# Optimization experiments

Measured on AMD Instinct MI355X. Metric: run time of the kernel, lower is better.

## Reference

```python
import jax, jax.numpy as jnp
import numpy as np
import math

D_MODEL = 1024
NUM_HEADS = 16
HEAD_DIM = D_MODEL // NUM_HEADS
B, T = 2, 2048


def _linear_params(key, d_in, d_out):
    kw, kb = jax.random.split(key)
    s = 1.0 / math.sqrt(d_in)
    W = jax.random.uniform(kw, (d_in, d_out), jnp.float32, -s, s)
    b = jax.random.uniform(kb, (d_out,), jnp.float32, -s, s)
    return W, b


def setup_inputs() -> dict:
    key = jax.random.key(0)
    ks = jax.random.split(key, 10)
    x_real = jax.random.normal(ks[0], (B, T, D_MODEL), jnp.float32)
    x_imag = jax.random.normal(ks[1], (B, T, D_MODEL), jnp.float32)
    Wqr, bqr = _linear_params(ks[2], D_MODEL, D_MODEL)
    Wqi, bqi = _linear_params(ks[3], D_MODEL, D_MODEL)
    Wkr, bkr = _linear_params(ks[4], D_MODEL, D_MODEL)
    Wki, bki = _linear_params(ks[5], D_MODEL, D_MODEL)
    Wvr, bvr = _linear_params(ks[6], D_MODEL, D_MODEL)
    Wvi, bvi = _linear_params(ks[7], D_MODEL, D_MODEL)
    Wor, bor = _linear_params(ks[8], D_MODEL, D_MODEL)
    Woi, boi = _linear_params(ks[9], D_MODEL, D_MODEL)
    return dict(x_real=x_real, x_imag=x_imag,
                Wqr=Wqr, bqr=bqr, Wqi=Wqi, bqi=bqi,
                Wkr=Wkr, bkr=bkr, Wki=Wki, bki=bki,
                Wvr=Wvr, bvr=bvr, Wvi=Wvi, bvi=bvi,
                Wor=Wor, bor=bor, Woi=Woi, boi=boi)


def _heads(x):
    # (B,T,C) -> (B,H,T,Dh)
    b, t, _ = x.shape
    return x.reshape(b, t, NUM_HEADS, HEAD_DIM).transpose(0, 2, 1, 3)


def reference(x_real, x_imag,
              Wqr, bqr, Wqi, bqi, Wkr, bkr, Wki, bki,
              Wvr, bvr, Wvi, bvi, Wor, bor, Woi, boi):
    b, t, c = x_real.shape
    # NOTE: first two qr/qi assignments in the torch forward are dead code;
    # effective math is below.
    qr = _heads(x_real @ Wqr + bqr)
    qi = _heads(x_imag @ Wqi + bqi)
    kr = _heads(x_real @ Wkr + bkr)
    ki = _heads(x_imag @ Wki + bki)
    vr = _heads(x_real @ Wvr + bvr)
    vi = _heads(x_imag @ Wvi + bvi)
    # Re(Q K^H) score: Qr*Kr + Qi*Ki, scaled
    score = (jnp.einsum('bhtd,bhsd->bhts', qr, kr)
             + jnp.einsum('bhtd,bhsd->bhts', qi, ki)) / math.sqrt(HEAD_DIM)
    causal = jnp.triu(jnp.ones((t, t), dtype=bool), k=1)  # True above diagonal
    score = jnp.where(causal[None, None], -jnp.inf, score)
    attn = jax.nn.softmax(score, axis=-1)
    out_r = jnp.einsum('bhts,bhsd->bhtd', attn, vr).transpose(0, 2, 1, 3).reshape(b, t, c)
    out_i = jnp.einsum('bhts,bhsd->bhtd', attn, vi).transpose(0, 2, 1, 3).reshape(b, t, c)
    final_r = out_r @ Wor + bor
    final_i = out_i @ Woi + boi
    return (final_r, final_i)
```

## Files before the change

### kernel.cpp

```cpp
#include <hip/hip_runtime.h>
#include <hip/hip_bf16.h>


typedef __attribute__((ext_vector_type(8))) __bf16 bf16x8;
typedef __attribute__((ext_vector_type(4))) float f32x4;
typedef unsigned short u16;

#define L2E 1.44269504088896340736f

__device__ __forceinline__ void gl2lds16(const void* g, void* l) {
  __builtin_amdgcn_global_load_lds(
      (const __attribute__((address_space(1))) unsigned int*)g,
      (__attribute__((address_space(3))) unsigned int*)l, 16, 0, 0);
}

__device__ __forceinline__ u16 f2bf(float f) {
  union { float f; unsigned u; } v;
  v.f = f;
  unsigned r = v.u + 0x7FFFu + ((v.u >> 16) & 1u);
  return (u16)(r >> 16);
}

__global__ void cvt_bf16(const float* __restrict__ in, u16* __restrict__ out, int n) {
  int stride = gridDim.x * blockDim.x * 4;
  for (int i = (blockIdx.x * blockDim.x + threadIdx.x) * 4; i < n; i += stride) {
    float4 v = *(const float4*)(in + i);
    ushort4 o;
    o.x = f2bf(v.x); o.y = f2bf(v.y); o.z = f2bf(v.z); o.w = f2bf(v.w);
    *(ushort4*)(out + i) = o;
  }
}

struct WPtrs { const float* w[8]; };

__global__ void cvt_w_t(WPtrs ptrs, u16* __restrict__ out) {
  __shared__ float tile[32][33];
  const float* W = ptrs.w[blockIdx.z];
  u16* o = out + ((size_t)blockIdx.z << 20);
  int tx = threadIdx.x & 31, ty = threadIdx.x >> 5;
  int bx = blockIdx.x * 32, by = blockIdx.y * 32;
#pragma unroll
  for (int k = 0; k < 4; k++) {
    int r = by + ty + k * 8;
    tile[ty + k * 8][tx] = W[(size_t)r * 1024 + bx + tx];
  }
  __syncthreads();
#pragma unroll
  for (int k = 0; k < 4; k++) {
    int n = bx + ty + k * 8;
    o[(size_t)n * 1024 + by + tx] = f2bf(tile[tx][ty + k * 8]);
  }
}

struct GemmArgs {
  const u16* A[6];
  const u16* Wt[6];
  const float* bias[6];
  void* dst[6];
  int off[6];
  float scale[6];
};

template <int MODE>
__global__ __launch_bounds__(256, 2) void gemm_bf16(GemmArgs args) {
  const int z = blockIdx.z;
  const u16* __restrict__ A = args.A[z];
  const u16* __restrict__ Bt = args.Wt[z];
  const float* __restrict__ bias = args.bias[z];
  const int brow = blockIdx.x * 128;
  const int bcol = blockIdx.y * 128;

  __shared__ u16 lA[2][128 * 32];
  __shared__ u16 lB[2][128 * 32];

  const int tid = threadIdx.x;
  const int w = tid >> 6, lane = tid & 63;
  const int wrow = (w >> 1) * 64, wcol = (w & 1) * 64;

  f32x4 acc[4][4] = {};

  auto stage = [&](int buf, int t) {
    int k0 = t * 32;
#pragma unroll
    for (int s = 0; s < 2; s++) {
      int q = w * 2 + s;
      int lr = q * 16 + (lane >> 2);
      int csrc = (lane & 3) ^ ((lr >> 1) & 3);
      gl2lds16(A + (size_t)(brow + lr) * 1024 + k0 + csrc * 8, &lA[buf][q * 512]);
    }
#pragma unroll
    for (int s = 0; s < 2; s++) {
      int q = w * 2 + s;
      int lr = q * 16 + (lane >> 2);
      int csrc = (lane & 3) ^ ((lr >> 1) & 3);
      gl2lds16(Bt + (size_t)(bcol + lr) * 1024 + k0 + csrc * 8, &lB[buf][q * 512]);
    }
  };

  stage(0, 0);
  __syncthreads();

  int buf = 0;
  for (int t = 0; t < 32; t++) {
    if (t + 1 < 32) stage(buf ^ 1, t + 1);
    bf16x8 a[4], b[4];
#pragma unroll
    for (int i = 0; i < 4; i++) {
      int row = wrow + i * 16 + (lane & 15);
      int cs = (lane >> 4) ^ ((row >> 1) & 3);
      a[i] = *(const bf16x8*)&lA[buf][row * 32 + cs * 8];
      int col = wcol + i * 16 + (lane & 15);
      int cs2 = (lane >> 4) ^ ((col >> 1) & 3);
      b[i] = *(const bf16x8*)&lB[buf][col * 32 + cs2 * 8];
    }
#pragma unroll
    for (int i = 0; i < 4; i++)
#pragma unroll
      for (int j = 0; j < 4; j++)
        acc[i][j] = __builtin_amdgcn_mfma_f32_16x16x32_bf16(a[i], b[j], acc[i][j], 0, 0, 0);
    __syncthreads();
    buf ^= 1;
  }

  const int off = args.off[z];
  const float scl = args.scale[z];
#pragma unroll
  for (int i = 0; i < 4; i++)
#pragma unroll
    for (int j = 0; j < 4; j++)
#pragma unroll
      for (int r = 0; r < 4; r++) {
        int grow = brow + wrow + i * 16 + (lane >> 4) * 4 + r;
        int gcol = bcol + wcol + j * 16 + (lane & 15);
        float v = (acc[i][j][r] + bias[gcol]) * scl;
        if (MODE == 0) {
          ((float*)args.dst[z])[(size_t)grow * 1024 + gcol] = v;
        } else {
          int bb = grow >> 11, tt = grow & 2047;
          int h = gcol >> 6, dh = gcol & 63;
          ((u16*)args.dst[z])[(((size_t)(bb * 16 + h) * 2048 + tt) << 7) + off + dh] = f2bf(v);
        }
      }
}

__global__ void transpose_v(const u16* __restrict__ Vc, u16* __restrict__ Vt) {
  __shared__ u16 tile[64 * 64];
  const int bh = blockIdx.z, t0 = blockIdx.x * 64, d0 = blockIdx.y * 64;
  const int tid = threadIdx.x;
  const int tl = tid >> 3, c = tid & 7;
#pragma unroll
  for (int hh = 0; hh < 2; hh++) {
    int t = tl + hh * 32;
    int sc = c ^ (t & 7) ^ ((t >> 3) & 7);
    *(bf16x8*)&tile[t * 64 + sc * 8] =
        *(const bf16x8*)&Vc[((size_t)bh * 2048 + t0 + t) * 128 + d0 + c * 8];
  }
  __syncthreads();
#pragma unroll
  for (int hh = 0; hh < 2; hh++) {
    int d = tl + hh * 32;
    bf16x8 v;
#pragma unroll
    for (int j = 0; j < 8; j++) {
      int t = c * 8 + j;
      int sc = (d >> 3) ^ (t & 7) ^ ((t >> 3) & 7);
      v[j] = ((const __bf16*)tile)[t * 64 + sc * 8 + (d & 7)];
    }
    *(bf16x8*)&Vt[((size_t)bh * 128 + d0 + d) * 2048 + t0 + c * 8] = v;
  }
}

__global__ __launch_bounds__(256, 2) void attn_kernel(
    const u16* __restrict__ Q, const u16* __restrict__ K, const u16* __restrict__ Vt,
    u16* __restrict__ Or, u16* __restrict__ Oi) {
  const int bh = blockIdx.x;
  const int ii = (int)gridDim.y - 1 - (int)blockIdx.y;
  const int tid = threadIdx.x, w = tid >> 6, lane = tid & 63;
  const int ql = lane & 15, hi = lane >> 4;
  const int b = bh >> 4, h = bh & 15;

  __shared__ u16 lK[2][64 * 128];
  __shared__ u16 lV[2][128 * 64];
  __shared__ u16 lP[4][16 * 64];

  const int qrow0 = ii * 64 + w * 16;
  const int q = qrow0 + ql;

  bf16x8 qf[4];
#pragma unroll
  for (int kk = 0; kk < 4; kk++)
    qf[kk] = *(const bf16x8*)(Q + ((size_t)bh * 2048 + q) * 128 + kk * 32 + hi * 8);

  f32x4 o[8] = {};
  float m = -__builtin_inff(), l = 0.f;

  const int ntiles = ii + 1;

  auto stageKV = [&](int buf, int jt) {
#pragma unroll
    for (int s = 0; s < 4; s++) {
      int seg = w * 4 + s;
      int srow = seg * 4 + (lane >> 4);
      int csrc = (lane & 15) ^ (srow & 15);
      gl2lds16(K + ((size_t)bh * 2048 + jt * 64 + srow) * 128 + csrc * 8, &lK[buf][seg * 512]);
    }
#pragma unroll
    for (int s = 0; s < 4; s++) {
      int seg = w * 4 + s;
      int dv = seg * 8 + (lane >> 3);
      int csrc = (lane & 7) ^ (dv & 7);
      gl2lds16(Vt + ((size_t)bh * 128 + dv) * 2048 + jt * 64 + csrc * 8, &lV[buf][seg * 512]);
    }
  };

  stageKV(0, 0);
  __syncthreads();

  int buf = 0;
  for (int jt = 0; jt < ntiles; jt++) {
    if (jt + 1 < ntiles) stageKV(buf ^ 1, jt + 1);

    f32x4 s[4] = {};
    __builtin_amdgcn_s_setprio(1);
#pragma unroll
    for (int kk = 0; kk < 4; kk++) {
#pragma unroll
      for (int j = 0; j < 4; j++) {
        int sl = j * 16 + ql;
        int cs = (kk * 4 + hi) ^ (sl & 15);
        bf16x8 kf = *(const bf16x8*)&lK[buf][sl * 128 + cs * 8];
        s[j] = __builtin_amdgcn_mfma_f32_16x16x32_bf16(kf, qf[kk], s[j], 0, 0, 0);
      }
    }
    __builtin_amdgcn_s_setprio(0);

    if (jt == ii) {
#pragma unroll
      for (int j = 0; j < 4; j++)
#pragma unroll
        for (int r = 0; r < 4; r++) {
          int kg = jt * 64 + j * 16 + hi * 4 + r;
          if (kg > q) s[j][r] = -__builtin_inff();
        }
    }

    float mx;
    {
      float a0 = fmaxf(fmaxf(s[0][0], s[0][1]), fmaxf(s[0][2], s[0][3]));
      float a1 = fmaxf(fmaxf(s[1][0], s[1][1]), fmaxf(s[1][2], s[1][3]));
      float a2 = fmaxf(fmaxf(s[2][0], s[2][1]), fmaxf(s[2][2], s[2][3]));
      float a3 = fmaxf(fmaxf(s[3][0], s[3][1]), fmaxf(s[3][2], s[3][3]));
      mx = fmaxf(fmaxf(a0, a1), fmaxf(a2, a3));
    }

    if (__any(mx > m + 8.f)) {
      mx = fmaxf(mx, __shfl_xor(mx, 16));
      mx = fmaxf(mx, __shfl_xor(mx, 32));
      float mn = fmaxf(m, mx);
      float alpha = exp2f((m - mn) * L2E);
      l *= alpha;
#pragma unroll
      for (int jv = 0; jv < 8; jv++) o[jv] *= alpha;
      m = mn;
    }

    uint2 pk[4];
#pragma unroll
    for (int j = 0; j < 4; j++) {
      float p0 = exp2f((s[j][0] - m) * L2E);
      float p1 = exp2f((s[j][1] - m) * L2E);
      float p2 = exp2f((s[j][2] - m) * L2E);
      float p3 = exp2f((s[j][3] - m) * L2E);
      l += (p0 + p1) + (p2 + p3);
      union { __bf16 hh[4]; uint2 u; } cv;
      cv.hh[0] = (__bf16)p0; cv.hh[1] = (__bf16)p1;
      cv.hh[2] = (__bf16)p2; cv.hh[3] = (__bf16)p3;
      pk[j] = cv.u;
    }

#pragma unroll
    for (int j = 0; j < 4; j++) {
      int byte_off = ql * 128 + ((j * 32 + hi * 8) ^ ((ql & 7) << 4));
      *(uint2*)((char*)&lP[w][0] + byte_off) = pk[j];
    }
    asm volatile("s_waitcnt lgkmcnt(0)" ::: "memory");
    __builtin_amdgcn_sched_barrier(0);

    __builtin_amdgcn_s_setprio(1);
#pragma unroll
    for (int kks = 0; kks < 2; kks++) {
      int pb = ql * 128 + ((kks * 64 + hi * 16) ^ ((ql & 7) << 4));
      bf16x8 pf = *(const bf16x8*)((char*)&lP[w][0] + pb);
#pragma unroll
      for (int jv = 0; jv < 8; jv++) {
        int dv = jv * 16 + ql;
        int cs = (kks * 4 + hi) ^ (dv & 7);
        bf16x8 vf = *(const bf16x8*)&lV[buf][dv * 64 + cs * 8];
        o[jv] = __builtin_amdgcn_mfma_f32_16x16x32_bf16(vf, pf, o[jv], 0, 0, 0);
      }
    }
    __builtin_amdgcn_s_setprio(0);

    __syncthreads();
    buf ^= 1;
  }

  l += __shfl_xor(l, 16);
  l += __shfl_xor(l, 32);
  float linv = 1.f / l;
  const size_t obase = ((size_t)b * 2048 + q) * 1024 + h * 64;
#pragma unroll
  for (int jv = 0; jv < 8; jv++) {
    ushort4 st;
    union { __bf16 hh[4]; ushort4 u; } cv;
    cv.hh[0] = (__bf16)(o[jv][0] * linv);
    cv.hh[1] = (__bf16)(o[jv][1] * linv);
    cv.hh[2] = (__bf16)(o[jv][2] * linv);
    cv.hh[3] = (__bf16)(o[jv][3] * linv);
    st = cv.u;
    u16* dst = (jv < 4) ? Or : Oi;
    *(ushort4*)(dst + obase + (jv & 3) * 16 + hi * 4) = st;
  }
}

extern "C" void kernel_launch(void* const* d_in, const int* in_sizes, int n_in,
                              void* d_out, int out_size, void* d_ws, size_t ws_size,
                              hipStream_t stream) {
  (void)in_sizes; (void)n_in; (void)out_size; (void)ws_size;

  const float* x_real = (const float*)d_in[0];
  const float* x_imag = (const float*)d_in[1];

  char* ws = (char*)d_ws;
  size_t off = 0;
  auto alloc = [&](size_t bytes) {
    void* p = ws + off;
    off += (bytes + 255) & ~(size_t)255;
    return p;
  };
  const size_t MK = 4096ull * 1024;
  u16* xr16 = (u16*)alloc(MK * 2);
  u16* xi16 = (u16*)alloc(MK * 2);
  u16* Wt   = (u16*)alloc(8ull * 1024 * 1024 * 2);
  u16* Qc   = (u16*)alloc(32ull * 2048 * 128 * 2);
  u16* Kc   = (u16*)alloc(32ull * 2048 * 128 * 2);
  u16* Vc   = (u16*)alloc(32ull * 2048 * 128 * 2);
  u16* Vt   = (u16*)alloc(32ull * 2048 * 128 * 2);
  u16* Or   = Vc;
  u16* Oi   = Vc + MK;

  cvt_bf16<<<2048, 256, 0, stream>>>(x_real, xr16, (int)MK);
  cvt_bf16<<<2048, 256, 0, stream>>>(x_imag, xi16, (int)MK);

  WPtrs wp;
  wp.w[0] = (const float*)d_in[2];
  wp.w[1] = (const float*)d_in[4];
  wp.w[2] = (const float*)d_in[6];
  wp.w[3] = (const float*)d_in[8];
  wp.w[4] = (const float*)d_in[10];
  wp.w[5] = (const float*)d_in[12];
  wp.w[6] = (const float*)d_in[14];
  wp.w[7] = (const float*)d_in[16];
  cvt_w_t<<<dim3(32, 32, 8), 256, 0, stream>>>(wp, Wt);

  GemmArgs pa{};
  const u16* xs[2] = {xr16, xi16};
  for (int z = 0; z < 6; z++) {
    pa.A[z] = xs[z & 1];
    pa.Wt[z] = Wt + (size_t)z * 1048576;
    pa.off[z] = (z & 1) * 64;
    pa.scale[z] = (z < 2) ? 0.125f : 1.0f;
  }
  pa.bias[0] = (const float*)d_in[3];
  pa.bias[1] = (const float*)d_in[5];
  pa.bias[2] = (const float*)d_in[7];
  pa.bias[3] = (const float*)d_in[9];
  pa.bias[4] = (const float*)d_in[11];
  pa.bias[5] = (const float*)d_in[13];
  pa.dst[0] = Qc; pa.dst[1] = Qc;
  pa.dst[2] = Kc; pa.dst[3] = Kc;
  pa.dst[4] = Vc; pa.dst[5] = Vc;
  gemm_bf16<1><<<dim3(32, 8, 6), 256, 0, stream>>>(pa);

  transpose_v<<<dim3(32, 2, 32), 256, 0, stream>>>(Vc, Vt);

  attn_kernel<<<dim3(32, 32), 256, 0, stream>>>(Qc, Kc, Vt, Or, Oi);

  GemmArgs fa{};
  fa.A[0] = Or; fa.A[1] = Oi;
  fa.Wt[0] = Wt + 6ull * 1048576;
  fa.Wt[1] = Wt + 7ull * 1048576;
  fa.bias[0] = (const float*)d_in[15];
  fa.bias[1] = (const float*)d_in[17];
  fa.dst[0] = (float*)d_out;
  fa.dst[1] = (float*)d_out + MK;
  fa.off[0] = 0; fa.off[1] = 0;
  fa.scale[0] = 1.0f; fa.scale[1] = 1.0f;
  gemm_bf16<0><<<dim3(32, 8, 2), 256, 0, stream>>>(fa);
}
```

Before: 188.6 us.

## Enlarge GEMM tiles to 256x256 with 512 threads and a 4-stage LDS pipeline

```diff
diff --git a/kernel.cpp b/kernel.cpp
--- a/kernel.cpp
+++ b/kernel.cpp
@@ -62,77 +62,114 @@
 };
 
 template <int MODE>
-__global__ __launch_bounds__(256, 2) void gemm_bf16(GemmArgs args) {
+__global__ __launch_bounds__(512, 2) void gemm256(GemmArgs args) {
   const int z = blockIdx.z;
   const u16* __restrict__ A = args.A[z];
   const u16* __restrict__ Bt = args.Wt[z];
   const float* __restrict__ bias = args.bias[z];
-  const int brow = blockIdx.x * 128;
-  const int bcol = blockIdx.y * 128;
-
-  __shared__ u16 lA[2][128 * 32];
-  __shared__ u16 lB[2][128 * 32];
+  const int brow = blockIdx.x * 256;
+  const int bcol = blockIdx.y * 256;
+
+  __shared__ u16 lA[4][256 * 32];
+  __shared__ u16 lB[4][256 * 32];
 
   const int tid = threadIdx.x;
   const int w = tid >> 6, lane = tid & 63;
-  const int wrow = (w >> 1) * 64, wcol = (w & 1) * 64;
-
-  f32x4 acc[4][4] = {};
-
-  auto stage = [&](int buf, int t) {
-    int k0 = t * 32;
+  const int ql = lane & 15, hi = lane >> 4;
+  const int wr = w >> 2, wc = w & 3;
+
+  f32x4 acc[8][4] = {};
+
+  auto stageA = [&](int kt, int buf) {
+    int k0 = kt * 32;
 #pragma unroll
     for (int s = 0; s < 2; s++) {
-      int q = w * 2 + s;
-      int lr = q * 16 + (lane >> 2);
-      int csrc = (lane & 3) ^ ((lr >> 1) & 3);
-      gl2lds16(A + (size_t)(brow + lr) * 1024 + k0 + csrc * 8, &lA[buf][q * 512]);
-    }
+      int seg = w + s * 8;
+      int r = seg * 16 + (lane >> 2);
+      int c = (lane & 3) ^ ((r >> 1) & 3);
+      gl2lds16(A + (size_t)(brow + r) * 1024 + k0 + c * 8, &lA[buf][seg * 512]);
+    }
+  };
+  auto stageB = [&](int kt, int buf) {
+    int k0 = kt * 32;
 #pragma unroll
     for (int s = 0; s < 2; s++) {
-      int q = w * 2 + s;
-      int lr = q * 16 + (lane >> 2);
-      int csrc = (lane & 3) ^ ((lr >> 1) & 3);
-      gl2lds16(Bt + (size_t)(bcol + lr) * 1024 + k0 + csrc * 8, &lB[buf][q * 512]);
+      int seg = w + s * 8;
+      int r = seg * 16 + (lane >> 2);
+      int c = (lane & 3) ^ ((r >> 1) & 3);
+      gl2lds16(Bt + (size_t)(bcol + r) * 1024 + k0 + c * 8, &lB[buf][seg * 512]);
     }
   };
 
-  stage(0, 0);
-  __syncthreads();
-
-  int buf = 0;
-  for (int t = 0; t < 32; t++) {
-    if (t + 1 < 32) stage(buf ^ 1, t + 1);
-    bf16x8 a[4], b[4];
+  stageA(0, 0); stageB(0, 0);
+  stageA(1, 1); stageB(1, 1);
+  stageA(2, 2); stageB(2, 2);
+  asm volatile("s_waitcnt vmcnt(8)" ::: "memory");
+  __builtin_amdgcn_s_barrier();
+
+  for (int kt = 0; kt < 32; kt++) {
+    const int buf = kt & 3;
+    const int pre = (kt + 3) & 3;
+    const bool more = (kt + 3) < 32;
+
+    bf16x8 b[4], a0[4], a1[4];
+
+    if (more) stageA(kt + 3, pre);
+#pragma unroll
+    for (int j = 0; j < 4; j++) {
+      int col = wc * 64 + j * 16 + ql;
+      int cs = hi ^ ((col >> 1) & 3);
+      b[j] = *(const bf16x8*)&lB[buf][col * 32 + cs * 8];
+    }
 #pragma unroll
     for (int i = 0; i < 4; i++) {
-      int row = wrow + i * 16 + (lane & 15);
-      int cs = (lane >> 4) ^ ((row >> 1) & 3);
-      a[i] = *(const bf16x8*)&lA[buf][row * 32 + cs * 8];
-      int col = wcol + i * 16 + (lane & 15);
-      int cs2 = (lane >> 4) ^ ((col >> 1) & 3);
-      b[i] = *(const bf16x8*)&lB[buf][col * 32 + cs2 * 8];
-    }
+      int row = wr * 128 + i * 16 + ql;
+      int cs = hi ^ ((row >> 1) & 3);
+      a0[i] = *(const bf16x8*)&lA[buf][row * 32 + cs * 8];
+    }
+    __builtin_amdgcn_s_setprio(1);
 #pragma unroll
     for (int i = 0; i < 4; i++)
 #pragma unroll
       for (int j = 0; j < 4; j++)
-        acc[i][j] = __builtin_amdgcn_mfma_f32_16x16x32_bf16(a[i], b[j], acc[i][j], 0, 0, 0);
-    __syncthreads();
-    buf ^= 1;
+        acc[i][j] = __builtin_amdgcn_mfma_f32_16x16x32_bf16(a0[i], b[j], acc[i][j], 0, 0, 0);
+    __builtin_amdgcn_s_setprio(0);
+    __builtin_amdgcn_s_barrier();
+
+    if (more) stageB(kt + 3, pre);
+#pragma unroll
+    for (int i = 0; i < 4; i++) {
+      int row = wr * 128 + 64 + i * 16 + ql;
+      int cs = hi ^ ((row >> 1) & 3);
+      a1[i] = *(const bf16x8*)&lA[buf][row * 32 + cs * 8];
+    }
+    __builtin_amdgcn_s_setprio(1);
+#pragma unroll
+    for (int i = 0; i < 4; i++)
+#pragma unroll
+      for (int j = 0; j < 4; j++)
+        acc[4 + i][j] = __builtin_amdgcn_mfma_f32_16x16x32_bf16(a1[i], b[j], acc[4 + i][j], 0, 0, 0);
+    __builtin_amdgcn_s_setprio(0);
+
+    if (kt <= 28)      asm volatile("s_waitcnt vmcnt(8)" ::: "memory");
+    else if (kt == 29) asm volatile("s_waitcnt vmcnt(4)" ::: "memory");
+    else if (kt == 30) asm volatile("s_waitcnt vmcnt(0)" ::: "memory");
+    __builtin_amdgcn_s_barrier();
   }
 
   const int off = args.off[z];
   const float scl = args.scale[z];
 #pragma unroll
-  for (int i = 0; i < 4; i++)
-#pragma unroll
-    for (int j = 0; j < 4; j++)
+  for (int ii = 0; ii < 8; ii++)
+#pragma unroll
+    for (int j = 0; j < 4; j++) {
+      int grow0 = brow + wr * 128 + (ii >> 2) * 64 + (ii & 3) * 16 + hi * 4;
+      int gcol = bcol + wc * 64 + j * 16 + ql;
+      float bv = bias[gcol];
 #pragma unroll
       for (int r = 0; r < 4; r++) {
-        int grow = brow + wrow + i * 16 + (lane >> 4) * 4 + r;
-        int gcol = bcol + wcol + j * 16 + (lane & 15);
-        float v = (acc[i][j][r] + bias[gcol]) * scl;
+        int grow = grow0 + r;
+        float v = (acc[ii][j][r] + bv) * scl;
         if (MODE == 0) {
           ((float*)args.dst[z])[(size_t)grow * 1024 + gcol] = v;
         } else {
@@ -141,6 +178,7 @@
           ((u16*)args.dst[z])[(((size_t)(bb * 16 + h) * 2048 + tt) << 7) + off + dh] = f2bf(v);
         }
       }
+    }
 }
 
 __global__ void transpose_v(const u16* __restrict__ Vc, u16* __restrict__ Vt) {
@@ -380,7 +418,7 @@
   pa.dst[0] = Qc; pa.dst[1] = Qc;
   pa.dst[2] = Kc; pa.dst[3] = Kc;
   pa.dst[4] = Vc; pa.dst[5] = Vc;
-  gemm_bf16<1><<<dim3(32, 8, 6), 256, 0, stream>>>(pa);
+  gemm256<1><<<dim3(16, 4, 6), 512, 0, stream>>>(pa);
 
   transpose_v<<<dim3(32, 2, 32), 256, 0, stream>>>(Vc, Vt);
 
@@ -396,5 +434,5 @@
   fa.dst[1] = (float*)d_out + MK;
   fa.off[0] = 0; fa.off[1] = 0;
   fa.scale[0] = 1.0f; fa.scale[1] = 1.0f;
-  gemm_bf16<0><<<dim3(32, 8, 2), 256, 0, stream>>>(fa);
-}
+  gemm256<0><<<dim3(16, 4, 2), 512, 0, stream>>>(fa);
+}
```

New measurement: 225.1 us. 1.19x slower.
